# Kernel optimization log

Measured on AMD Instinct MI355X. Metric: run time of the kernel, lower is better.

The kernel has to match this reference:

```python
import jax, jax.numpy as jnp
import numpy as np

B, N, D = 8, 2048, 512
S = 4096  # max_swaps


def setup_inputs() -> dict:
    key = jax.random.key(0)
    ks = jax.random.split(key, 5)
    h = jax.random.normal(ks[0], (B, N, D), dtype=jnp.float32)
    indices = jax.random.randint(ks[1], (B, S, 4), 0, N, dtype=jnp.int64)
    # MLP params (Linear stores weight as (out,in) in torch; we keep (in,out) and matmul)
    W1 = jax.random.normal(ks[2], (4 * D, D), dtype=jnp.float32) * (1.0 / np.sqrt(4 * D))
    b1 = jnp.zeros((D,), dtype=jnp.float32)
    W2 = jax.random.normal(ks[3], (D, D // 2), dtype=jnp.float32) * (1.0 / np.sqrt(D))
    b2 = jnp.zeros((D // 2,), dtype=jnp.float32)
    W3 = jax.random.normal(ks[4], (D // 2, 1), dtype=jnp.float32) * (1.0 / np.sqrt(D // 2))
    b3 = jnp.zeros((1,), dtype=jnp.float32)
    return {"h": h, "indices": indices, "W1": W1, "b1": b1, "W2": W2, "b2": b2, "W3": W3, "b3": b3}


def reference(h, indices, W1, b1, W2, b2, W3, b3):
    # h: (B, N, D); indices: (B, S, 4) node ids per swap
    swap_emb = jnp.take_along_axis(h[:, None, :, :], indices[..., None].astype(jnp.int32),
                                   axis=2)  # broadcast-gather -> (B, S, 4, D)
    # equivalently: h[batch_idx, indices]; implemented as per-batch gather
    swap_emb = jax.vmap(lambda hb, ib: hb[ib])(h, indices)  # (B, S, 4, D)
    swap_feats = swap_emb.reshape(h.shape[0], indices.shape[1], -1)  # (B, S, 4D)
    x = jax.nn.gelu(swap_feats @ W1 + b1, approximate=False)
    x = jax.nn.gelu(x @ W2 + b2, approximate=False)
    scores = (x @ W3 + b3)[..., 0]  # (B, S)
    rates = jax.nn.softplus(scores)
    return rates
```

## Files before the change

### kernel.cpp

```cpp
#include <hip/hip_runtime.h>
#include <math.h>

#define BATCH 8
#define NNODES 2048
#define DDIM 512
#define SWAPS 4096
#define M_TOTAL (BATCH * SWAPS)
#define KD DDIM
#define K2 DDIM
#define N2 (DDIM / 2)

typedef __attribute__((ext_vector_type(8))) __bf16 bf16x8;
typedef __attribute__((ext_vector_type(4))) float f32x4;
typedef __attribute__((ext_vector_type(8))) unsigned short us8;
typedef unsigned short ushort_t;

__device__ __forceinline__ float gelu_fast(float x) {
    const float u = 0.7978845608028654f * x * fmaf(0.044715f * x, x, 1.0f);
    const float e = __expf(-2.0f * fabsf(u));
    float t = (1.0f - e) / (1.0f + e);
    t = copysignf(t, u);
    return 0.5f * x * (1.0f + t);
}
__device__ __forceinline__ float softplus_f(float x) {
    return fmaxf(x, 0.0f) + log1pf(expf(-fabsf(x)));
}
__device__ __forceinline__ unsigned short f2bf(float f) {
    unsigned int u = __builtin_bit_cast(unsigned int, f);
    u += 0x7FFFu + ((u >> 16) & 1u);
    return (unsigned short)(u >> 16);
}
__device__ __forceinline__ float bf2f(unsigned short s) {
    return __builtin_bit_cast(float, (unsigned int)s << 16);
}
__device__ __forceinline__ void glds16(const void* g, void* l) {
    __builtin_amdgcn_global_load_lds(
        (const __attribute__((address_space(1))) void*)g,
        (__attribute__((address_space(3))) void*)l, 16, 0, 0);
}

__global__ __launch_bounds__(256) void convert_kernel(
    const float* __restrict__ h, const float* __restrict__ W1,
    const float* __restrict__ W2, ushort_t* __restrict__ h_bf,
    ushort_t* __restrict__ W1pt, ushort_t* __restrict__ W2f)
{
    const int bid = blockIdx.x;
    const int tid = threadIdx.x;
    if (bid < 4096) {
        const size_t i = ((size_t)bid * 256 + tid) * 8;
        float4 v0 = *(const float4*)(h + i);
        float4 v1 = *(const float4*)(h + i + 4);
        us8 o;
        o[0] = f2bf(v0.x); o[1] = f2bf(v0.y); o[2] = f2bf(v0.z); o[3] = f2bf(v0.w);
        o[4] = f2bf(v1.x); o[5] = f2bf(v1.y); o[6] = f2bf(v1.z); o[7] = f2bf(v1.w);
        *(us8*)(h_bf + i) = o;
    } else if (bid < 4096 + 256) {
        __shared__ ushort_t sT[64][72];
        const int tb = bid - 4096;
        const int kt = tb >> 3, nt = tb & 7;
        const int kl = tid >> 4;
        const int n4 = (tid & 15) * 4;
        #pragma unroll
        for (int p = 0; p < 4; ++p) {
            const int k_local = p * 16 + kl;
            float4 v = *(const float4*)(W1 + (size_t)(kt * 64 + k_local) * 512
                                        + nt * 64 + n4);
            sT[n4 + 0][k_local] = f2bf(v.x);
            sT[n4 + 1][k_local] = f2bf(v.y);
            sT[n4 + 2][k_local] = f2bf(v.z);
            sT[n4 + 3][k_local] = f2bf(v.w);
        }
        __syncthreads();
        const int n_local = tid >> 2, ch = tid & 3;
        const int j = (kt >> 3) * 512 + nt * 64 + n_local;
        const int d0 = (kt & 7) * 64 + ch * 16;
        us8 o0, o1;
        #pragma unroll
        for (int e = 0; e < 8; ++e) { o0[e] = sT[n_local][ch * 16 + e];
                                      o1[e] = sT[n_local][ch * 16 + 8 + e]; }
        *(us8*)(W1pt + (size_t)j * KD + d0)     = o0;
        *(us8*)(W1pt + (size_t)j * KD + d0 + 8) = o1;
    } else {
        size_t e = ((size_t)(bid - 4352) * 256 + tid) * 4;
        const int k = (int)(e >> 8), n = (int)(e & 255);
        const int kc = k >> 5, quad = (k >> 3) & 3, pos = k & 7;
        const size_t base = (size_t)kc * 8192 + quad * 8 + pos;
        float4 v = *(const float4*)(W2 + e);
        W2f[base + (size_t)(n + 0) * 32] = f2bf(v.x);
        W2f[base + (size_t)(n + 1) * 32] = f2bf(v.y);
        W2f[base + (size_t)(n + 2) * 32] = f2bf(v.z);
        W2f[base + (size_t)(n + 3) * 32] = f2bf(v.w);
    }
}

__global__ __launch_bounds__(256, 4) void gemm1_dense(
    const ushort_t* __restrict__ h_bf, const ushort_t* __restrict__ W1pt,
    ushort_t* __restrict__ P2)
{
    __shared__ __align__(16) char smem[32768];

    const int tid = threadIdx.x;
    const int w = tid >> 6, lane = tid & 63;
    const int quad = lane >> 4, l16 = lane & 15;
    const int wr = w >> 1, wc = w & 1;

    const int bid = blockIdx.x;
    const int xcd = bid & 7;
    const int r = bid >> 3;
    const int m0 = xcd * NNODES + (r & 15) * 128;
    const int n0 = (r >> 4) * 128;

    const int row0 = tid >> 2, sub = tid & 3;
    const int cg = (sub - (row0 >> 1)) & 3;
    const ushort_t* bA0 = h_bf + (size_t)(m0 + row0) * KD + cg * 8;
    const ushort_t* bA1 = h_bf + (size_t)(m0 + row0 + 64) * KD + cg * 8;
    const ushort_t* bB0 = W1pt + (size_t)(n0 + row0) * KD + cg * 8;
    const ushort_t* bB1 = W1pt + (size_t)(n0 + row0 + 64) * KD + cg * 8;

    int pa[4], pb[4];
    #pragma unroll
    for (int i = 0; i < 4; ++i) {
        const int rA = wr * 64 + i * 16 + l16;
        const int rB = wc * 64 + i * 16 + l16;
        pa[i] = rA * 64 + (((quad + (rA >> 1)) & 3) * 16);
        pb[i] = 8192 + rB * 64 + (((quad + (rB >> 1)) & 3) * 16);
    }

    f32x4 acc[4][4] = {};

    auto stage = [&](int kt, int half) {
        const int oo = kt * 32;
        char* base = smem + half * 16384;
        glds16(bA0 + oo, base + w * 1024);
        glds16(bA1 + oo, base + 4096 + w * 1024);
        glds16(bB0 + oo, base + 8192 + w * 1024);
        glds16(bB1 + oo, base + 12288 + w * 1024);
    };
    auto compute = [&](int half) {
        const char* base = smem + half * 16384;
        bf16x8 af[4], bfr[4];
        #pragma unroll
        for (int i = 0; i < 4; ++i) {
            af[i]  = *(const bf16x8*)(base + pa[i]);
            bfr[i] = *(const bf16x8*)(base + pb[i]);
        }
        #pragma unroll
        for (int i = 0; i < 4; ++i)
            #pragma unroll
            for (int jj = 0; jj < 4; ++jj)
                acc[i][jj] = __builtin_amdgcn_mfma_f32_16x16x32_bf16(
                    af[i], bfr[jj], acc[i][jj], 0, 0, 0);
    };

    for (int kt = 0; kt < 16; kt += 2) {
        stage(kt, 0);
        stage(kt + 1, 1);
        __syncthreads();
        compute(0);
        compute(1);
        __syncthreads();
    }

    #pragma unroll
    for (int jj = 0; jj < 4; ++jj) {
        const int j = n0 + wc * 64 + jj * 16 + l16;
        const int sg = j >> 9, nh = j & 511;
        const size_t base = ((size_t)(xcd * 2 + (nh >> 8)) * NNODES) * 1024
                          + (size_t)(sg << 8) + (nh & 255);
        #pragma unroll
        for (int i = 0; i < 4; ++i) {
            f32x4 v = acc[i][jj];
            #pragma unroll
            for (int rr = 0; rr < 4; ++rr) {
                const int node = (m0 + wr * 64 + i * 16 + quad * 4 + rr) & (NNODES - 1);
                P2[base + (size_t)node * 1024] = f2bf(v[rr]);
            }
        }
    }
}

__global__ __launch_bounds__(256, 4) void fused_tail(
    const ushort_t* __restrict__ P2, const int* __restrict__ idx,
    const float* __restrict__ b1, const ushort_t* __restrict__ W2f,
    const float* __restrict__ b2, const float* __restrict__ W3,
    const float* __restrict__ b3, float* __restrict__ out)
{
    __shared__ __align__(16) char smem[33280];

    const int tid = threadIdx.x;
    const int w = tid >> 6, lane = tid & 63;
    const int quad = lane >> 4, l16 = lane & 15;

    const int bid = blockIdx.x;
    const int b = bid & 7;
    const int m0 = b * SWAPS + (bid >> 3) * 32;

    {
        const int row = tid >> 3;
        const int ws  = tid & 7;
        const int ap  = ws & 3;
        const int ncs = ws >> 2;
        const int acg = (ap - (row >> 1)) & 3;
        const int4 iv = *(const int4*)(idx + (size_t)(m0 + row) * 4);
        const ushort_t* Pr = P2 + (size_t)(b * 2 + ncs) * NNODES * 1024;
        const ushort_t* p0 = Pr + (size_t)iv.x * 1024 + 0 * 256;
        const ushort_t* p1 = Pr + (size_t)iv.y * 1024 + 1 * 256;
        const ushort_t* p2 = Pr + (size_t)iv.z * 1024 + 2 * 256;
        const ushort_t* p3 = Pr + (size_t)iv.w * 1024 + 3 * 256;
        #pragma unroll 4
        for (int it = 0; it < 8; ++it) {
            const int kc = ncs * 8 + it;
            const int pos0 = it * 32 + acg * 8;
            us8 v0 = *(const us8*)(p0 + pos0);
            us8 v1 = *(const us8*)(p1 + pos0);
            us8 v2 = *(const us8*)(p2 + pos0);
            us8 v3 = *(const us8*)(p3 + pos0);
            const float* bp = b1 + ncs * 256 + pos0;
            float4 ba = *(const float4*)bp;
            float4 bb = *(const float4*)(bp + 4);
            float s[8] = { ba.x, ba.y, ba.z, ba.w, bb.x, bb.y, bb.z, bb.w };
            #pragma unroll
            for (int e = 0; e < 8; ++e)
                s[e] += bf2f(v0[e]) + bf2f(v1[e]) + bf2f(v2[e]) + bf2f(v3[e]);
            us8 o;
            #pragma unroll
            for (int e = 0; e < 8; ++e) o[e] = f2bf(gelu_fast(s[e]));
            *(us8*)(smem + kc * 2048 + row * 64 + ap * 16) = o;
        }
    }
    __syncthreads();

    const int cg = w;
    int paRow[2];
    #pragma unroll
    for (int i = 0; i < 2; ++i) {
        const int rA = i * 16 + l16;
        paRow[i] = rA * 64 + (((quad + (rA >> 1)) & 3) * 16);
    }
    const ushort_t* Bbase = W2f + (size_t)(cg * 64 + l16) * 32 + quad * 8;

    f32x4 acc[2][4] = {};

    #pragma unroll 2
    for (int kc = 0; kc < 16; ++kc) {
        bf16x8 af0 = *(const bf16x8*)(smem + kc * 2048 + paRow[0]);
        bf16x8 af1 = *(const bf16x8*)(smem + kc * 2048 + paRow[1]);
        #pragma unroll
        for (int jf = 0; jf < 4; ++jf) {
            bf16x8 bfr = *(const bf16x8*)(Bbase + (size_t)kc * 8192 + jf * 512);
            acc[0][jf] = __builtin_amdgcn_mfma_f32_16x16x32_bf16(af0, bfr, acc[0][jf], 0, 0, 0);
            acc[1][jf] = __builtin_amdgcn_mfma_f32_16x16x32_bf16(af1, bfr, acc[1][jf], 0, 0, 0);
        }
    }

    float part[2][4] = {};
    #pragma unroll
    for (int jf = 0; jf < 4; ++jf) {
        const int n = cg * 64 + jf * 16 + l16;
        const float w3 = W3[n];
        const float bb2 = b2[n];
        #pragma unroll
        for (int i = 0; i < 2; ++i) {
            f32x4 v = acc[i][jf];
            #pragma unroll
            for (int rr = 0; rr < 4; ++rr)
                part[i][rr] = fmaf(gelu_fast(v[rr] + bb2), w3, part[i][rr]);
        }
    }
    #pragma unroll
    for (int off = 1; off < 16; off <<= 1)
        #pragma unroll
        for (int i = 0; i < 2; ++i)
            #pragma unroll
            for (int rr = 0; rr < 4; ++rr)
                part[i][rr] += __shfl_xor(part[i][rr], off);

    float* red = (float*)(smem + 32768);
    if (l16 == 0) {
        #pragma unroll
        for (int i = 0; i < 2; ++i)
            #pragma unroll
            for (int rr = 0; rr < 4; ++rr)
                red[cg * 32 + i * 16 + quad * 4 + rr] = part[i][rr];
    }
    __syncthreads();
    if (tid < 32) {
        const float v = red[tid] + red[32 + tid] + red[64 + tid] + red[96 + tid];
        out[m0 + tid] = softplus_f(v + b3[0]);
    }
}

extern "C" void kernel_launch(void* const* d_in, const int* in_sizes, int n_in,
                              void* d_out, int out_size, void* d_ws, size_t ws_size,
                              hipStream_t stream) {
    const float* h   = (const float*)d_in[0];
    const int*   idx = (const int*)d_in[1];
    const float* W1  = (const float*)d_in[2];
    const float* b1  = (const float*)d_in[3];
    const float* W2  = (const float*)d_in[4];
    const float* b2  = (const float*)d_in[5];
    const float* W3  = (const float*)d_in[6];
    const float* b3  = (const float*)d_in[7];
    float* out = (float*)d_out;

    char* ws = (char*)d_ws;
    ushort_t* P2    = (ushort_t*)ws;
    ushort_t* h_bf  = (ushort_t*)(ws + (64u << 20));
    ushort_t* W1pt  = (ushort_t*)(ws + (80u << 20));
    ushort_t* W2f   = (ushort_t*)(ws + (82u << 20));

    convert_kernel<<<4480, 256, 0, stream>>>(h, W1, W2, h_bf, W1pt, W2f);
    gemm1_dense<<<2048, 256, 0, stream>>>(h_bf, W1pt, P2);
    fused_tail<<<1024, 256, 0, stream>>>(P2, idx, b1, W2f, b2, W3, b3, out);
}
```

Before: 169.0 us.

## Merge three kernels into one cooperative persistent kernel with grid syncs

Replaces the convert, GEMM1 and fused-tail launches with a single cooperative kernel that loops over virtual blocks and separates the phases with grid-wide syncs and thread fences. The goal is to remove launch gaps and tail effects between the three kernels. In exchange the grid is capped at 1024 resident blocks, so each block runs several tiles serially, and the grid barriers add their own cost. Extra __syncthreads were added so shared memory can be reused safely between iterations.

```diff
diff --git a/kernel.cpp b/kernel.cpp
--- a/kernel.cpp
+++ b/kernel.cpp
@@ -1,5 +1,8 @@
 #include <hip/hip_runtime.h>
+#include <hip/hip_cooperative_groups.h>
 #include <math.h>
+
+namespace cg = cooperative_groups;
 
 #define BATCH 8
 #define NNODES 2048
@@ -39,254 +42,260 @@
         (__attribute__((address_space(3))) void*)l, 16, 0, 0);
 }
 
-__global__ __launch_bounds__(256) void convert_kernel(
-    const float* __restrict__ h, const float* __restrict__ W1,
-    const float* __restrict__ W2, ushort_t* __restrict__ h_bf,
-    ushort_t* __restrict__ W1pt, ushort_t* __restrict__ W2f)
+__global__ __launch_bounds__(256, 4) void mega(
+    const float* __restrict__ h, const int* __restrict__ idx,
+    const float* __restrict__ W1, const float* __restrict__ b1,
+    const float* __restrict__ W2, const float* __restrict__ b2,
+    const float* __restrict__ W3, const float* __restrict__ b3,
+    float* __restrict__ out, ushort_t* __restrict__ P2,
+    ushort_t* __restrict__ h_bf, ushort_t* __restrict__ W1pt,
+    ushort_t* __restrict__ W2f)
 {
-    const int bid = blockIdx.x;
+    __shared__ __align__(16) char smem[33280];
+    cg::grid_group gg = cg::this_grid();
     const int tid = threadIdx.x;
-    if (bid < 4096) {
-        const size_t i = ((size_t)bid * 256 + tid) * 8;
-        float4 v0 = *(const float4*)(h + i);
-        float4 v1 = *(const float4*)(h + i + 4);
-        us8 o;
-        o[0] = f2bf(v0.x); o[1] = f2bf(v0.y); o[2] = f2bf(v0.z); o[3] = f2bf(v0.w);
-        o[4] = f2bf(v1.x); o[5] = f2bf(v1.y); o[6] = f2bf(v1.z); o[7] = f2bf(v1.w);
-        *(us8*)(h_bf + i) = o;
-    } else if (bid < 4096 + 256) {
-        __shared__ ushort_t sT[64][72];
-        const int tb = bid - 4096;
-        const int kt = tb >> 3, nt = tb & 7;
-        const int kl = tid >> 4;
-        const int n4 = (tid & 15) * 4;
-        #pragma unroll
-        for (int p = 0; p < 4; ++p) {
-            const int k_local = p * 16 + kl;
-            float4 v = *(const float4*)(W1 + (size_t)(kt * 64 + k_local) * 512
-                                        + nt * 64 + n4);
-            sT[n4 + 0][k_local] = f2bf(v.x);
-            sT[n4 + 1][k_local] = f2bf(v.y);
-            sT[n4 + 2][k_local] = f2bf(v.z);
-            sT[n4 + 3][k_local] = f2bf(v.w);
-        }
-        __syncthreads();
-        const int n_local = tid >> 2, ch = tid & 3;
-        const int j = (kt >> 3) * 512 + nt * 64 + n_local;
-        const int d0 = (kt & 7) * 64 + ch * 16;
-        us8 o0, o1;
-        #pragma unroll
-        for (int e = 0; e < 8; ++e) { o0[e] = sT[n_local][ch * 16 + e];
-                                      o1[e] = sT[n_local][ch * 16 + 8 + e]; }
-        *(us8*)(W1pt + (size_t)j * KD + d0)     = o0;
-        *(us8*)(W1pt + (size_t)j * KD + d0 + 8) = o1;
-    } else {
-        size_t e = ((size_t)(bid - 4352) * 256 + tid) * 4;
-        const int k = (int)(e >> 8), n = (int)(e & 255);
-        const int kc = k >> 5, quad = (k >> 3) & 3, pos = k & 7;
-        const size_t base = (size_t)kc * 8192 + quad * 8 + pos;
-        float4 v = *(const float4*)(W2 + e);
-        W2f[base + (size_t)(n + 0) * 32] = f2bf(v.x);
-        W2f[base + (size_t)(n + 1) * 32] = f2bf(v.y);
-        W2f[base + (size_t)(n + 2) * 32] = f2bf(v.z);
-        W2f[base + (size_t)(n + 3) * 32] = f2bf(v.w);
-    }
-}
-
-__global__ __launch_bounds__(256, 4) void gemm1_dense(
-    const ushort_t* __restrict__ h_bf, const ushort_t* __restrict__ W1pt,
-    ushort_t* __restrict__ P2)
-{
-    __shared__ __align__(16) char smem[32768];
-
-    const int tid = threadIdx.x;
-    const int w = tid >> 6, lane = tid & 63;
-    const int quad = lane >> 4, l16 = lane & 15;
-    const int wr = w >> 1, wc = w & 1;
-
-    const int bid = blockIdx.x;
-    const int xcd = bid & 7;
-    const int r = bid >> 3;
-    const int m0 = xcd * NNODES + (r & 15) * 128;
-    const int n0 = (r >> 4) * 128;
-
-    const int row0 = tid >> 2, sub = tid & 3;
-    const int cg = (sub - (row0 >> 1)) & 3;
-    const ushort_t* bA0 = h_bf + (size_t)(m0 + row0) * KD + cg * 8;
-    const ushort_t* bA1 = h_bf + (size_t)(m0 + row0 + 64) * KD + cg * 8;
-    const ushort_t* bB0 = W1pt + (size_t)(n0 + row0) * KD + cg * 8;
-    const ushort_t* bB1 = W1pt + (size_t)(n0 + row0 + 64) * KD + cg * 8;
-
-    int pa[4], pb[4];
-    #pragma unroll
-    for (int i = 0; i < 4; ++i) {
-        const int rA = wr * 64 + i * 16 + l16;
-        const int rB = wc * 64 + i * 16 + l16;
-        pa[i] = rA * 64 + (((quad + (rA >> 1)) & 3) * 16);
-        pb[i] = 8192 + rB * 64 + (((quad + (rB >> 1)) & 3) * 16);
-    }
-
-    f32x4 acc[4][4] = {};
-
-    auto stage = [&](int kt, int half) {
-        const int oo = kt * 32;
-        char* base = smem + half * 16384;
-        glds16(bA0 + oo, base + w * 1024);
-        glds16(bA1 + oo, base + 4096 + w * 1024);
-        glds16(bB0 + oo, base + 8192 + w * 1024);
-        glds16(bB1 + oo, base + 12288 + w * 1024);
-    };
-    auto compute = [&](int half) {
-        const char* base = smem + half * 16384;
-        bf16x8 af[4], bfr[4];
-        #pragma unroll
-        for (int i = 0; i < 4; ++i) {
-            af[i]  = *(const bf16x8*)(base + pa[i]);
-            bfr[i] = *(const bf16x8*)(base + pb[i]);
-        }
-        #pragma unroll
-        for (int i = 0; i < 4; ++i)
-            #pragma unroll
-            for (int jj = 0; jj < 4; ++jj)
-                acc[i][jj] = __builtin_amdgcn_mfma_f32_16x16x32_bf16(
-                    af[i], bfr[jj], acc[i][jj], 0, 0, 0);
-    };
-
-    for (int kt = 0; kt < 16; kt += 2) {
-        stage(kt, 0);
-        stage(kt + 1, 1);
-        __syncthreads();
-        compute(0);
-        compute(1);
-        __syncthreads();
-    }
-
-    #pragma unroll
-    for (int jj = 0; jj < 4; ++jj) {
-        const int j = n0 + wc * 64 + jj * 16 + l16;
-        const int sg = j >> 9, nh = j & 511;
-        const size_t base = ((size_t)(xcd * 2 + (nh >> 8)) * NNODES) * 1024
-                          + (size_t)(sg << 8) + (nh & 255);
-        #pragma unroll
-        for (int i = 0; i < 4; ++i) {
-            f32x4 v = acc[i][jj];
-            #pragma unroll
-            for (int rr = 0; rr < 4; ++rr) {
-                const int node = (m0 + wr * 64 + i * 16 + quad * 4 + rr) & (NNODES - 1);
-                P2[base + (size_t)node * 1024] = f2bf(v[rr]);
-            }
+
+    for (int vb = blockIdx.x; vb < 4480; vb += gridDim.x) {
+        if (vb < 4096) {
+            const size_t i = ((size_t)vb * 256 + tid) * 8;
+            float4 v0 = *(const float4*)(h + i);
+            float4 v1 = *(const float4*)(h + i + 4);
+            us8 o;
+            o[0] = f2bf(v0.x); o[1] = f2bf(v0.y); o[2] = f2bf(v0.z); o[3] = f2bf(v0.w);
+            o[4] = f2bf(v1.x); o[5] = f2bf(v1.y); o[6] = f2bf(v1.z); o[7] = f2bf(v1.w);
+            *(us8*)(h_bf + i) = o;
+        } else if (vb < 4096 + 256) {
+            ushort_t (*sT)[72] = (ushort_t(*)[72])smem;
+            const int tb = vb - 4096;
+            const int kt = tb >> 3, nt = tb & 7;
+            const int kl = tid >> 4;
+            const int n4 = (tid & 15) * 4;
+            #pragma unroll
+            for (int p = 0; p < 4; ++p) {
+                const int k_local = p * 16 + kl;
+                float4 v = *(const float4*)(W1 + (size_t)(kt * 64 + k_local) * 512
+                                            + nt * 64 + n4);
+                sT[n4 + 0][k_local] = f2bf(v.x);
+                sT[n4 + 1][k_local] = f2bf(v.y);
+                sT[n4 + 2][k_local] = f2bf(v.z);
+                sT[n4 + 3][k_local] = f2bf(v.w);
+            }
+            __syncthreads();
+            const int n_local = tid >> 2, ch = tid & 3;
+            const int j = (kt >> 3) * 512 + nt * 64 + n_local;
+            const int d0 = (kt & 7) * 64 + ch * 16;
+            us8 o0, o1;
+            #pragma unroll
+            for (int e = 0; e < 8; ++e) { o0[e] = sT[n_local][ch * 16 + e];
+                                          o1[e] = sT[n_local][ch * 16 + 8 + e]; }
+            *(us8*)(W1pt + (size_t)j * KD + d0)     = o0;
+            *(us8*)(W1pt + (size_t)j * KD + d0 + 8) = o1;
+            __syncthreads();
+        } else {
+            size_t e = ((size_t)(vb - 4352) * 256 + tid) * 4;
+            const int k = (int)(e >> 8), n = (int)(e & 255);
+            const int kc = k >> 5, quad = (k >> 3) & 3, pos = k & 7;
+            const size_t base = (size_t)kc * 8192 + quad * 8 + pos;
+            float4 v = *(const float4*)(W2 + e);
+            W2f[base + (size_t)(n + 0) * 32] = f2bf(v.x);
+            W2f[base + (size_t)(n + 1) * 32] = f2bf(v.y);
+            W2f[base + (size_t)(n + 2) * 32] = f2bf(v.z);
+            W2f[base + (size_t)(n + 3) * 32] = f2bf(v.w);
         }
     }
-}
-
-__global__ __launch_bounds__(256, 4) void fused_tail(
-    const ushort_t* __restrict__ P2, const int* __restrict__ idx,
-    const float* __restrict__ b1, const ushort_t* __restrict__ W2f,
-    const float* __restrict__ b2, const float* __restrict__ W3,
-    const float* __restrict__ b3, float* __restrict__ out)
-{
-    __shared__ __align__(16) char smem[33280];
-
-    const int tid = threadIdx.x;
-    const int w = tid >> 6, lane = tid & 63;
-    const int quad = lane >> 4, l16 = lane & 15;
-
-    const int bid = blockIdx.x;
-    const int b = bid & 7;
-    const int m0 = b * SWAPS + (bid >> 3) * 32;
+
+    __threadfence();
+    gg.sync();
+    __threadfence();
 
     {
-        const int row = tid >> 3;
-        const int ws  = tid & 7;
-        const int ap  = ws & 3;
-        const int ncs = ws >> 2;
-        const int acg = (ap - (row >> 1)) & 3;
-        const int4 iv = *(const int4*)(idx + (size_t)(m0 + row) * 4);
-        const ushort_t* Pr = P2 + (size_t)(b * 2 + ncs) * NNODES * 1024;
-        const ushort_t* p0 = Pr + (size_t)iv.x * 1024 + 0 * 256;
-        const ushort_t* p1 = Pr + (size_t)iv.y * 1024 + 1 * 256;
-        const ushort_t* p2 = Pr + (size_t)iv.z * 1024 + 2 * 256;
-        const ushort_t* p3 = Pr + (size_t)iv.w * 1024 + 3 * 256;
-        #pragma unroll 4
-        for (int it = 0; it < 8; ++it) {
-            const int kc = ncs * 8 + it;
-            const int pos0 = it * 32 + acg * 8;
-            us8 v0 = *(const us8*)(p0 + pos0);
-            us8 v1 = *(const us8*)(p1 + pos0);
-            us8 v2 = *(const us8*)(p2 + pos0);
-            us8 v3 = *(const us8*)(p3 + pos0);
-            const float* bp = b1 + ncs * 256 + pos0;
-            float4 ba = *(const float4*)bp;
-            float4 bb = *(const float4*)(bp + 4);
-            float s[8] = { ba.x, ba.y, ba.z, ba.w, bb.x, bb.y, bb.z, bb.w };
-            #pragma unroll
-            for (int e = 0; e < 8; ++e)
-                s[e] += bf2f(v0[e]) + bf2f(v1[e]) + bf2f(v2[e]) + bf2f(v3[e]);
-            us8 o;
-            #pragma unroll
-            for (int e = 0; e < 8; ++e) o[e] = f2bf(gelu_fast(s[e]));
-            *(us8*)(smem + kc * 2048 + row * 64 + ap * 16) = o;
+        const int w = tid >> 6, lane = tid & 63;
+        const int quad = lane >> 4, l16 = lane & 15;
+        const int wr = w >> 1, wc = w & 1;
+        const int row0 = tid >> 2, sub = tid & 3;
+        const int cgk = (sub - (row0 >> 1)) & 3;
+
+        for (int vb = blockIdx.x; vb < 2048; vb += gridDim.x) {
+            const int xcd = vb & 7;
+            const int r = vb >> 3;
+            const int m0 = xcd * NNODES + (r & 15) * 128;
+            const int n0 = (r >> 4) * 128;
+
+            const ushort_t* bA0 = h_bf + (size_t)(m0 + row0) * KD + cgk * 8;
+            const ushort_t* bA1 = h_bf + (size_t)(m0 + row0 + 64) * KD + cgk * 8;
+            const ushort_t* bB0 = W1pt + (size_t)(n0 + row0) * KD + cgk * 8;
+            const ushort_t* bB1 = W1pt + (size_t)(n0 + row0 + 64) * KD + cgk * 8;
+
+            int pa[4], pb[4];
+            #pragma unroll
+            for (int i = 0; i < 4; ++i) {
+                const int rA = wr * 64 + i * 16 + l16;
+                const int rB = wc * 64 + i * 16 + l16;
+                pa[i] = rA * 64 + (((quad + (rA >> 1)) & 3) * 16);
+                pb[i] = 8192 + rB * 64 + (((quad + (rB >> 1)) & 3) * 16);
+            }
+
+            f32x4 acc[4][4] = {};
+
+            auto stage = [&](int kt, int half) {
+                const int oo = kt * 32;
+                char* base = smem + half * 16384;
+                glds16(bA0 + oo, base + w * 1024);
+                glds16(bA1 + oo, base + 4096 + w * 1024);
+                glds16(bB0 + oo, base + 8192 + w * 1024);
+                glds16(bB1 + oo, base + 12288 + w * 1024);
+            };
+            auto compute = [&](int half) {
+                const char* base = smem + half * 16384;
+                bf16x8 af[4], bfr[4];
+                #pragma unroll
+                for (int i = 0; i < 4; ++i) {
+                    af[i]  = *(const bf16x8*)(base + pa[i]);
+                    bfr[i] = *(const bf16x8*)(base + pb[i]);
+                }
+                #pragma unroll
+                for (int i = 0; i < 4; ++i)
+                    #pragma unroll
+                    for (int jj = 0; jj < 4; ++jj)
+                        acc[i][jj] = __builtin_amdgcn_mfma_f32_16x16x32_bf16(
+                            af[i], bfr[jj], acc[i][jj], 0, 0, 0);
+            };
+
+            for (int kt = 0; kt < 16; kt += 2) {
+                stage(kt, 0);
+                stage(kt + 1, 1);
+                __syncthreads();
+                compute(0);
+                compute(1);
+                __syncthreads();
+            }
+
+            #pragma unroll
+            for (int jj = 0; jj < 4; ++jj) {
+                const int j = n0 + wc * 64 + jj * 16 + l16;
+                const int sg = j >> 9, nh = j & 511;
+                const size_t base = ((size_t)(xcd * 2 + (nh >> 8)) * NNODES) * 1024
+                                  + (size_t)(sg << 8) + (nh & 255);
+                #pragma unroll
+                for (int i = 0; i < 4; ++i) {
+                    f32x4 v = acc[i][jj];
+                    #pragma unroll
+                    for (int rr = 0; rr < 4; ++rr) {
+                        const int node = (m0 + wr * 64 + i * 16 + quad * 4 + rr) & (NNODES - 1);
+                        P2[base + (size_t)node * 1024] = f2bf(v[rr]);
+                    }
+                }
+            }
         }
     }
-    __syncthreads();
-
-    const int cg = w;
-    int paRow[2];
-    #pragma unroll
-    for (int i = 0; i < 2; ++i) {
-        const int rA = i * 16 + l16;
-        paRow[i] = rA * 64 + (((quad + (rA >> 1)) & 3) * 16);
-    }
-    const ushort_t* Bbase = W2f + (size_t)(cg * 64 + l16) * 32 + quad * 8;
-
-    f32x4 acc[2][4] = {};
-
-    #pragma unroll 2
-    for (int kc = 0; kc < 16; ++kc) {
-        bf16x8 af0 = *(const bf16x8*)(smem + kc * 2048 + paRow[0]);
-        bf16x8 af1 = *(const bf16x8*)(smem + kc * 2048 + paRow[1]);
-        #pragma unroll
-        for (int jf = 0; jf < 4; ++jf) {
-            bf16x8 bfr = *(const bf16x8*)(Bbase + (size_t)kc * 8192 + jf * 512);
-            acc[0][jf] = __builtin_amdgcn_mfma_f32_16x16x32_bf16(af0, bfr, acc[0][jf], 0, 0, 0);
-            acc[1][jf] = __builtin_amdgcn_mfma_f32_16x16x32_bf16(af1, bfr, acc[1][jf], 0, 0, 0);
+
+    __threadfence();
+    gg.sync();
+    __threadfence();
+
+    {
+        const int w = tid >> 6, lane = tid & 63;
+        const int quad = lane >> 4, l16 = lane & 15;
+
+        for (int vb = blockIdx.x; vb < 1024; vb += gridDim.x) {
+            const int b = vb & 7;
+            const int m0 = b * SWAPS + (vb >> 3) * 32;
+
+            {
+                const int row = tid >> 3;
+                const int ws  = tid & 7;
+                const int ap  = ws & 3;
+                const int ncs = ws >> 2;
+                const int acg = (ap - (row >> 1)) & 3;
+                const int4 iv = *(const int4*)(idx + (size_t)(m0 + row) * 4);
+                const ushort_t* Pr = P2 + (size_t)(b * 2 + ncs) * NNODES * 1024;
+                const ushort_t* p0 = Pr + (size_t)iv.x * 1024 + 0 * 256;
+                const ushort_t* p1 = Pr + (size_t)iv.y * 1024 + 1 * 256;
+                const ushort_t* p2 = Pr + (size_t)iv.z * 1024 + 2 * 256;
+                const ushort_t* p3 = Pr + (size_t)iv.w * 1024 + 3 * 256;
+                #pragma unroll 4
+                for (int it = 0; it < 8; ++it) {
+                    const int kc = ncs * 8 + it;
+                    const int pos0 = it * 32 + acg * 8;
+                    us8 v0 = *(const us8*)(p0 + pos0);
+                    us8 v1 = *(const us8*)(p1 + pos0);
+                    us8 v2 = *(const us8*)(p2 + pos0);
+                    us8 v3 = *(const us8*)(p3 + pos0);
+                    const float* bp = b1 + ncs * 256 + pos0;
+                    float4 ba = *(const float4*)bp;
+                    float4 bb = *(const float4*)(bp + 4);
+                    float s[8] = { ba.x, ba.y, ba.z, ba.w, bb.x, bb.y, bb.z, bb.w };
+                    #pragma unroll
+                    for (int e = 0; e < 8; ++e)
+                        s[e] += bf2f(v0[e]) + bf2f(v1[e]) + bf2f(v2[e]) + bf2f(v3[e]);
+                    us8 o;
+                    #pragma unroll
+                    for (int e = 0; e < 8; ++e) o[e] = f2bf(gelu_fast(s[e]));
+                    *(us8*)(smem + kc * 2048 + row * 64 + ap * 16) = o;
+                }
+            }
+            __syncthreads();
+
+            const int cgw = w;
+            int paRow[2];
+            #pragma unroll
+            for (int i = 0; i < 2; ++i) {
+                const int rA = i * 16 + l16;
+                paRow[i] = rA * 64 + (((quad + (rA >> 1)) & 3) * 16);
+            }
+            const ushort_t* Bbase = W2f + (size_t)(cgw * 64 + l16) * 32 + quad * 8;
+
+            f32x4 acc[2][4] = {};
+
+            #pragma unroll 2
+            for (int kc = 0; kc < 16; ++kc) {
+                bf16x8 af0 = *(const bf16x8*)(smem + kc * 2048 + paRow[0]);
+                bf16x8 af1 = *(const bf16x8*)(smem + kc * 2048 + paRow[1]);
+                #pragma unroll
+                for (int jf = 0; jf < 4; ++jf) {
+                    bf16x8 bfr = *(const bf16x8*)(Bbase + (size_t)kc * 8192 + jf * 512);
+                    acc[0][jf] = __builtin_amdgcn_mfma_f32_16x16x32_bf16(af0, bfr, acc[0][jf], 0, 0, 0);
+                    acc[1][jf] = __builtin_amdgcn_mfma_f32_16x16x32_bf16(af1, bfr, acc[1][jf], 0, 0, 0);
+                }
+            }
+
+            float part[2][4] = {};
+            #pragma unroll
+            for (int jf = 0; jf < 4; ++jf) {
+                const int n = cgw * 64 + jf * 16 + l16;
+                const float w3 = W3[n];
+                const float bb2 = b2[n];
+                #pragma unroll
+                for (int i = 0; i < 2; ++i) {
+                    f32x4 v = acc[i][jf];
+                    #pragma unroll
+                    for (int rr = 0; rr < 4; ++rr)
+                        part[i][rr] = fmaf(gelu_fast(v[rr] + bb2), w3, part[i][rr]);
+                }
+            }
+            #pragma unroll
+            for (int off = 1; off < 16; off <<= 1)
+                #pragma unroll
+                for (int i = 0; i < 2; ++i)
+                    #pragma unroll
+                    for (int rr = 0; rr < 4; ++rr)
+                        part[i][rr] += __shfl_xor(part[i][rr], off);
+
+            float* red = (float*)(smem + 32768);
+            if (l16 == 0) {
+                #pragma unroll
+                for (int i = 0; i < 2; ++i)
+                    #pragma unroll
+                    for (int rr = 0; rr < 4; ++rr)
+                        red[cgw * 32 + i * 16 + quad * 4 + rr] = part[i][rr];
+            }
+            __syncthreads();
+            if (tid < 32) {
+                const float v = red[tid] + red[32 + tid] + red[64 + tid] + red[96 + tid];
+                out[m0 + tid] = softplus_f(v + b3[0]);
+            }
+            __syncthreads();
         }
-    }
-
-    float part[2][4] = {};
-    #pragma unroll
-    for (int jf = 0; jf < 4; ++jf) {
-        const int n = cg * 64 + jf * 16 + l16;
-        const float w3 = W3[n];
-        const float bb2 = b2[n];
-        #pragma unroll
-        for (int i = 0; i < 2; ++i) {
-            f32x4 v = acc[i][jf];
-            #pragma unroll
-            for (int rr = 0; rr < 4; ++rr)
-                part[i][rr] = fmaf(gelu_fast(v[rr] + bb2), w3, part[i][rr]);
-        }
-    }
-    #pragma unroll
-    for (int off = 1; off < 16; off <<= 1)
-        #pragma unroll
-        for (int i = 0; i < 2; ++i)
-            #pragma unroll
-            for (int rr = 0; rr < 4; ++rr)
-                part[i][rr] += __shfl_xor(part[i][rr], off);
-
-    float* red = (float*)(smem + 32768);
-    if (l16 == 0) {
-        #pragma unroll
-        for (int i = 0; i < 2; ++i)
-            #pragma unroll
-            for (int rr = 0; rr < 4; ++rr)
-                red[cg * 32 + i * 16 + quad * 4 + rr] = part[i][rr];
-    }
-    __syncthreads();
-    if (tid < 32) {
-        const float v = red[tid] + red[32 + tid] + red[64 + tid] + red[96 + tid];
-        out[m0 + tid] = softplus_f(v + b3[0]);
     }
 }
 
@@ -309,7 +318,23 @@
     ushort_t* W1pt  = (ushort_t*)(ws + (80u << 20));
     ushort_t* W2f   = (ushort_t*)(ws + (82u << 20));
 
-    convert_kernel<<<4480, 256, 0, stream>>>(h, W1, W2, h_bf, W1pt, W2f);
-    gemm1_dense<<<2048, 256, 0, stream>>>(h_bf, W1pt, P2);
-    fused_tail<<<1024, 256, 0, stream>>>(P2, idx, b1, W2f, b2, W3, b3, out);
-}
+    static int s_grid = 0;
+    if (s_grid == 0) {
+        int nb = 0;
+        if (hipOccupancyMaxActiveBlocksPerMultiprocessor(&nb, mega, 256, 0)
+                != hipSuccess || nb < 1)
+            nb = 1;
+        int g = nb * 256;
+        if (g > 1024) g = 1024;
+        g &= ~7;
+        if (g < 8) g = 8;
+        s_grid = g;
+    }
+
+    void* args[] = { (void*)&h, (void*)&idx, (void*)&W1, (void*)&b1,
+                     (void*)&W2, (void*)&b2, (void*)&W3, (void*)&b3,
+                     (void*)&out, (void*)&P2, (void*)&h_bf, (void*)&W1pt,
+                     (void*)&W2f };
+    hipLaunchCooperativeKernel((const void*)mega, dim3(s_grid), dim3(256),
+                               args, 0, stream);
+}
```

Result: slower. 510.4 us (+201.9%).
